# Optimization experiments

Measured on AMD Instinct MI355X. Metric: run time of the kernel, lower is better.

## Reference

```python
import jax, jax.numpy as jnp
import numpy as np

# LABEL2ID assumed: O=0, B-PERSON=1, I-PERSON=2 (standard tagset ordering)
B_ID = 1
I_ID = 2
SMOOTH = 1e-5
B_WEIGHT = 3.0
I_END_WEIGHT = 2.5
CONTEXT_WEIGHT = 1.5
N_TOKENS = 8388608
NUM_CLASSES = 9


def setup_inputs() -> dict:
    key = jax.random.key(0)
    k1, k2 = jax.random.split(key)
    inputs = jax.random.normal(k1, (N_TOKENS, NUM_CLASSES), dtype=jnp.float32)
    targets = jax.random.randint(k2, (N_TOKENS,), 0, NUM_CLASSES)
    return {"inputs": inputs, "targets": targets}


def _boundary_weights(t):
    # base weight 1; B-PERSON -> b_weight
    w = jnp.ones(t.shape, jnp.float32)
    w = jnp.where(t == B_ID, B_WEIGHT, w)
    # I-PERSON followed by non-I-PERSON -> i_end_weight
    # (torch pads shifted with the last element, so the final I is never flagged here)
    nxt_dup = jnp.concatenate([t[1:], t[-1:]])
    w = jnp.where((t == I_ID) & (nxt_dup != I_ID), I_END_WEIGHT, w)
    # token immediately before a B-PERSON -> context_weight (overwrites prior weights,
    # matching torch's later scatter assignment; index -1 for a leading B is filtered out)
    nxt0 = jnp.concatenate([t[1:], jnp.zeros((1,), t.dtype)])
    w = jnp.where(nxt0 == B_ID, CONTEXT_WEIGHT, w)
    return w


def reference(inputs, targets):
    probs = jax.nn.softmax(inputs, axis=1)                      # [N, C]
    one_hot = jax.nn.one_hot(targets, NUM_CLASSES, dtype=jnp.float32)
    w = _boundary_weights(targets)[:, None]                     # [N, 1]
    intersection = jnp.sum(probs * one_hot * w, axis=0)         # [C]
    denominator = jnp.sum(probs * w, axis=0) + jnp.sum(one_hot * w, axis=0)
    dice_coef = (2.0 * intersection + SMOOTH) / (denominator + SMOOTH)
    return 1.0 - dice_coef.mean()
```

## Files before the change

### kernel.cpp

```cpp
#include <hip/hip_runtime.h>

#define NC 9
#define BLOCK 256
#define TPT 4
#define CHUNK (BLOCK * TPT)
#define GRID 2048


__global__ __launch_bounds__(BLOCK) void dice_partial(
    const float* __restrict__ logits,
    const int*   __restrict__ targets,
    float*       __restrict__ partials,
    int n)
{
    float sWP[NC], sI[NC], sOH[NC];
    #pragma unroll
    for (int c = 0; c < NC; ++c) { sWP[c] = 0.f; sI[c] = 0.f; sOH[c] = 0.f; }

    const int tid = threadIdx.x;
    const int nChunks = (n + CHUNK - 1) / CHUNK;

    for (int chunk = blockIdx.x; chunk < nChunks; chunk += gridDim.x) {
        const int base = chunk * CHUNK + tid * TPT;

        if (base + TPT <= n) {
            const float4* g4 = reinterpret_cast<const float4*>(logits + (size_t)base * NC);
            float f[TPT * NC];
            #pragma unroll
            for (int k = 0; k < 9; ++k) {
                const float4 q = g4[k];
                f[4 * k]     = q.x;
                f[4 * k + 1] = q.y;
                f[4 * k + 2] = q.z;
                f[4 * k + 3] = q.w;
            }
            const int4 t4 = *reinterpret_cast<const int4*>(targets + base);
            int tg[TPT];
            tg[0] = t4.x; tg[1] = t4.y; tg[2] = t4.z; tg[3] = t4.w;
            const int  tExtra = (base + TPT < n) ? targets[base + TPT] : 0;
            const bool lastIsGlobalEnd = (base + TPT == n);

            #pragma unroll
            for (int j = 0; j < TPT; ++j) {
                const int  t    = tg[j];
                const bool last = (j == TPT - 1) && lastIsGlobalEnd;
                const int  tn   = (j < TPT - 1) ? tg[j + 1] : tExtra;

                float w = 1.0f;
                if (t == 1) w = 3.0f;
                const int nxt_dup = last ? t : tn;
                if (t == 2 && nxt_dup != 2) w = 2.5f;
                if (!last && tn == 1) w = 1.5f;

                float v[NC];
                float s = 0.f;
                #pragma unroll
                for (int c = 0; c < NC; ++c) { v[c] = __expf(f[j * NC + c]); s += v[c]; }
                const float inv = __builtin_amdgcn_rcpf(s);

                #pragma unroll
                for (int c = 0; c < NC; ++c) {
                    const float p   = v[c] * inv;
                    const bool  hit = (t == c);
                    sWP[c] += w * p;
                    sI[c]  += hit ? w * p : 0.f;
                    sOH[c] += hit ? w : 0.f;
                }
            }
        } else {
            for (int j = 0; j < TPT; ++j) {
                const int a = base + j;
                if (a >= n) break;
                const int  t    = targets[a];
                const bool last = (a == n - 1);
                const int  tn   = last ? 0 : targets[a + 1];

                float w = 1.0f;
                if (t == 1) w = 3.0f;
                const int nxt_dup = last ? t : tn;
                if (t == 2 && nxt_dup != 2) w = 2.5f;
                if (!last && tn == 1) w = 1.5f;

                float v[NC];
                float s = 0.f;
                #pragma unroll
                for (int c = 0; c < NC; ++c) { v[c] = __expf(logits[(size_t)a * NC + c]); s += v[c]; }
                const float inv = __builtin_amdgcn_rcpf(s);

                #pragma unroll
                for (int c = 0; c < NC; ++c) {
                    const float p   = v[c] * inv;
                    const bool  hit = (t == c);
                    sWP[c] += w * p;
                    sI[c]  += hit ? w * p : 0.f;
                    sOH[c] += hit ? w : 0.f;
                }
            }
        }
    }

    #pragma unroll
    for (int off = 32; off; off >>= 1) {
        #pragma unroll
        for (int c = 0; c < NC; ++c) {
            sWP[c] += __shfl_down(sWP[c], off);
            sI[c]  += __shfl_down(sI[c], off);
            sOH[c] += __shfl_down(sOH[c], off);
        }
    }

    __shared__ float red[4][32];
    const int lane = tid & 63;
    const int wid  = tid >> 6;
    if (lane == 0) {
        #pragma unroll
        for (int c = 0; c < NC; ++c) {
            red[wid][c]      = sWP[c];
            red[wid][9 + c]  = sI[c];
            red[wid][18 + c] = sOH[c];
        }
    }
    __syncthreads();
    if (tid < 27) {
        partials[blockIdx.x * 32 + tid] =
            red[0][tid] + red[1][tid] + red[2][tid] + red[3][tid];
    }
}

__global__ __launch_bounds__(1024) void dice_reduce(
    const float* __restrict__ partials,
    float*       __restrict__ out,
    int nblocks)
{
    const int c = threadIdx.x & 31;
    const int r = threadIdx.x >> 5;
    float s = 0.f;
    if (c < 27) {
        for (int b = r; b < nblocks; b += 32)
            s += partials[b * 32 + c];
    }
    __shared__ float acc[32][33];
    acc[r][c] = s;
    __syncthreads();

    __shared__ float A[32];
    if (threadIdx.x < 32) {
        float tot = 0.f;
        #pragma unroll
        for (int k = 0; k < 32; ++k) tot += acc[k][threadIdx.x];
        A[threadIdx.x] = tot;
    }
    __syncthreads();
    if (threadIdx.x == 0) {
        float dsum = 0.f;
        #pragma unroll
        for (int cc = 0; cc < NC; ++cc) {
            const float inter = A[9 + cc];
            const float den   = A[cc] + A[18 + cc];
            dsum += (2.f * inter + 1e-5f) / (den + 1e-5f);
        }
        out[0] = 1.f - dsum * (1.f / 9.f);
    }
}

extern "C" void kernel_launch(void* const* d_in, const int* in_sizes, int n_in,
                              void* d_out, int out_size, void* d_ws, size_t ws_size,
                              hipStream_t stream)
{
    const float* logits   = (const float*)d_in[0];
    const int*   targets  = (const int*)d_in[1];
    float*       out      = (float*)d_out;
    float*       partials = (float*)d_ws;
    const int n = in_sizes[1];

    const int nChunks = (n + CHUNK - 1) / CHUNK;
    const int grid = nChunks < GRID ? nChunks : GRID;
    dice_partial<<<grid, BLOCK, 0, stream>>>(logits, targets, partials, n);
    dice_reduce<<<1, 1024, 0, stream>>>(partials, out, grid);
}
```

Baseline: 78.82 us.

## Stage logits through LDS with coalesced loads and register double-buffering

Each block is reduced to a single 64-thread wavefront that loads 256 tokens' logits as perfectly coalesced float4s (lane-strided) into registers, stores them to LDS, then reads them back per-thread in token-contiguous order. The next chunk's global loads are issued before computing the current chunk, giving software prefetch in two register sets. This replaces strided per-thread 144-byte vector loads, which coalesce poorly, and removes the cross-wave shared reduction and barrier. It trades higher register pressure and fewer threads per block, which may lower latency hiding, and the grid stays capped at 2048 single-wave blocks.

```diff
diff --git a/kernel.cpp b/kernel.cpp
--- a/kernel.cpp
+++ b/kernel.cpp
@@ -1,101 +1,121 @@
 #include <hip/hip_runtime.h>
 
 #define NC 9
-#define BLOCK 256
-#define TPT 4
-#define CHUNK (BLOCK * TPT)
+#define TPW 256
+#define F4PW (TPW * NC / 4)
 #define GRID 2048
 
 
-__global__ __launch_bounds__(BLOCK) void dice_partial(
+__global__ __launch_bounds__(64) void dice_partial(
     const float* __restrict__ logits,
     const int*   __restrict__ targets,
     float*       __restrict__ partials,
     int n)
 {
+    __shared__ __align__(16) float4 buf[2][F4PW];
+    __shared__ float red[32];
+
     float sWP[NC], sI[NC], sOH[NC];
     #pragma unroll
     for (int c = 0; c < NC; ++c) { sWP[c] = 0.f; sI[c] = 0.f; sOH[c] = 0.f; }
 
-    const int tid = threadIdx.x;
-    const int nChunks = (n + CHUNK - 1) / CHUNK;
+    const int l = threadIdx.x;
+    const int G = gridDim.x;
+    const int nFull = n / TPW;
 
-    for (int chunk = blockIdx.x; chunk < nChunks; chunk += gridDim.x) {
-        const int base = chunk * CHUNK + tid * TPT;
+    const float4* gbase = reinterpret_cast<const float4*>(logits);
 
-        if (base + TPT <= n) {
-            const float4* g4 = reinterpret_cast<const float4*>(logits + (size_t)base * NC);
-            float f[TPT * NC];
-            #pragma unroll
-            for (int k = 0; k < 9; ++k) {
-                const float4 q = g4[k];
-                f[4 * k]     = q.x;
-                f[4 * k + 1] = q.y;
-                f[4 * k + 2] = q.z;
-                f[4 * k + 3] = q.w;
-            }
-            const int4 t4 = *reinterpret_cast<const int4*>(targets + base);
-            int tg[TPT];
-            tg[0] = t4.x; tg[1] = t4.y; tg[2] = t4.z; tg[3] = t4.w;
-            const int  tExtra = (base + TPT < n) ? targets[base + TPT] : 0;
-            const bool lastIsGlobalEnd = (base + TPT == n);
+    float4 tA0,tA1,tA2,tA3,tA4,tA5,tA6,tA7,tA8;
+    float4 tB0,tB1,tB2,tB3,tB4,tB5,tB6,tB7,tB8;
 
-            #pragma unroll
-            for (int j = 0; j < TPT; ++j) {
-                const int  t    = tg[j];
-                const bool last = (j == TPT - 1) && lastIsGlobalEnd;
-                const int  tn   = (j < TPT - 1) ? tg[j + 1] : tExtra;
+#define LOADT(dst, c)  do { const float4* g4 = gbase + (size_t)(c) * F4PW; \
+        dst##0 = g4[0*64+l]; dst##1 = g4[1*64+l]; dst##2 = g4[2*64+l]; \
+        dst##3 = g4[3*64+l]; dst##4 = g4[4*64+l]; dst##5 = g4[5*64+l]; \
+        dst##6 = g4[6*64+l]; dst##7 = g4[7*64+l]; dst##8 = g4[8*64+l]; } while(0)
 
-                float w = 1.0f;
-                if (t == 1) w = 3.0f;
-                const int nxt_dup = last ? t : tn;
-                if (t == 2 && nxt_dup != 2) w = 2.5f;
-                if (!last && tn == 1) w = 1.5f;
+#define STORET(p, src) do { float4* B = &buf[p][0]; \
+        B[0*64+l]=src##0; B[1*64+l]=src##1; B[2*64+l]=src##2; \
+        B[3*64+l]=src##3; B[4*64+l]=src##4; B[5*64+l]=src##5; \
+        B[6*64+l]=src##6; B[7*64+l]=src##7; B[8*64+l]=src##8; } while(0)
 
-                float v[NC];
-                float s = 0.f;
-                #pragma unroll
-                for (int c = 0; c < NC; ++c) { v[c] = __expf(f[j * NC + c]); s += v[c]; }
-                const float inv = __builtin_amdgcn_rcpf(s);
+#define COMPUTE(p, cch) do {                                                  \
+        float f[4 * NC];                                                      \
+        _Pragma("unroll")                                                     \
+        for (int k = 0; k < 9; ++k) {                                         \
+            const float4 q = buf[p][l * 9 + k];                               \
+            f[4*k] = q.x; f[4*k+1] = q.y; f[4*k+2] = q.z; f[4*k+3] = q.w;     \
+        }                                                                     \
+        const int tok0 = (cch) * TPW + l * 4;                                 \
+        const int4 t4 = *reinterpret_cast<const int4*>(targets + tok0);       \
+        int tg[4]; tg[0]=t4.x; tg[1]=t4.y; tg[2]=t4.z; tg[3]=t4.w;            \
+        const int  tExtra = (tok0 + 4 < n) ? targets[tok0 + 4] : 0;           \
+        const bool lastIsEnd = (tok0 + 4 == n);                               \
+        _Pragma("unroll")                                                     \
+        for (int j = 0; j < 4; ++j) {                                         \
+            const int  t    = tg[j];                                          \
+            const bool last = (j == 3) && lastIsEnd;                          \
+            const int  tn   = (j < 3) ? tg[j + 1] : tExtra;                   \
+            float w = 1.0f;                                                   \
+            if (t == 1) w = 3.0f;                                             \
+            const int nxt_dup = last ? t : tn;                                \
+            if (t == 2 && nxt_dup != 2) w = 2.5f;                             \
+            if (!last && tn == 1) w = 1.5f;                                   \
+            float v[NC]; float s = 0.f;                                       \
+            _Pragma("unroll")                                                 \
+            for (int c = 0; c < NC; ++c) { v[c] = __expf(f[j*NC+c]); s += v[c]; } \
+            const float inv = __builtin_amdgcn_rcpf(s);                       \
+            _Pragma("unroll")                                                 \
+            for (int c = 0; c < NC; ++c) {                                    \
+                const float p_ = v[c] * inv;                                  \
+                const bool hit = (t == c);                                    \
+                sWP[c] += w * p_;                                             \
+                sI[c]  += hit ? w * p_ : 0.f;                                 \
+                sOH[c] += hit ? w : 0.f;                                      \
+            }                                                                 \
+        }                                                                     \
+    } while(0)
 
-                #pragma unroll
-                for (int c = 0; c < NC; ++c) {
-                    const float p   = v[c] * inv;
-                    const bool  hit = (t == c);
-                    sWP[c] += w * p;
-                    sI[c]  += hit ? w * p : 0.f;
-                    sOH[c] += hit ? w : 0.f;
-                }
-            }
-        } else {
-            for (int j = 0; j < TPT; ++j) {
-                const int a = base + j;
-                if (a >= n) break;
-                const int  t    = targets[a];
-                const bool last = (a == n - 1);
-                const int  tn   = last ? 0 : targets[a + 1];
+    int c0 = blockIdx.x;
+    if (c0 < nFull) LOADT(tA, c0);
 
-                float w = 1.0f;
-                if (t == 1) w = 3.0f;
-                const int nxt_dup = last ? t : tn;
-                if (t == 2 && nxt_dup != 2) w = 2.5f;
-                if (!last && tn == 1) w = 1.5f;
+    while (c0 < nFull) {
+        STORET(0, tA);
+        {
+            const int c1 = c0 + G;
+            if (c1 < nFull) LOADT(tB, c1);
+            COMPUTE(0, c0);
+            c0 = c1;
+        }
+        if (c0 >= nFull) break;
+        STORET(1, tB);
+        {
+            const int c2 = c0 + G;
+            if (c2 < nFull) LOADT(tA, c2);
+            COMPUTE(1, c0);
+            c0 = c2;
+        }
+    }
 
-                float v[NC];
-                float s = 0.f;
-                #pragma unroll
-                for (int c = 0; c < NC; ++c) { v[c] = __expf(logits[(size_t)a * NC + c]); s += v[c]; }
-                const float inv = __builtin_amdgcn_rcpf(s);
-
-                #pragma unroll
-                for (int c = 0; c < NC; ++c) {
-                    const float p   = v[c] * inv;
-                    const bool  hit = (t == c);
-                    sWP[c] += w * p;
-                    sI[c]  += hit ? w * p : 0.f;
-                    sOH[c] += hit ? w : 0.f;
-                }
-            }
+    for (int a = nFull * TPW + blockIdx.x * 64 + l; a < n; a += G * 64) {
+        const int  t    = targets[a];
+        const bool last = (a == n - 1);
+        const int  tn   = last ? 0 : targets[a + 1];
+        float w = 1.0f;
+        if (t == 1) w = 3.0f;
+        const int nxt_dup = last ? t : tn;
+        if (t == 2 && nxt_dup != 2) w = 2.5f;
+        if (!last && tn == 1) w = 1.5f;
+        float v[NC]; float s = 0.f;
+        #pragma unroll
+        for (int c = 0; c < NC; ++c) { v[c] = __expf(logits[(size_t)a * NC + c]); s += v[c]; }
+        const float inv = __builtin_amdgcn_rcpf(s);
+        #pragma unroll
+        for (int c = 0; c < NC; ++c) {
+            const float p = v[c] * inv;
+            const bool hit = (t == c);
+            sWP[c] += w * p;
+            sI[c]  += hit ? w * p : 0.f;
+            sOH[c] += hit ? w : 0.f;
         }
     }
 
@@ -109,22 +129,16 @@
         }
     }
 
-    __shared__ float red[4][32];
-    const int lane = tid & 63;
-    const int wid  = tid >> 6;
-    if (lane == 0) {
+    if (l == 0) {
         #pragma unroll
         for (int c = 0; c < NC; ++c) {
-            red[wid][c]      = sWP[c];
-            red[wid][9 + c]  = sI[c];
-            red[wid][18 + c] = sOH[c];
+            red[c]      = sWP[c];
+            red[9 + c]  = sI[c];
+            red[18 + c] = sOH[c];
         }
     }
-    __syncthreads();
-    if (tid < 27) {
-        partials[blockIdx.x * 32 + tid] =
-            red[0][tid] + red[1][tid] + red[2][tid] + red[3][tid];
-    }
+    __builtin_amdgcn_s_waitcnt(0);
+    if (l < 27) partials[blockIdx.x * 32 + l] = red[l];
 }
 
 __global__ __launch_bounds__(1024) void dice_reduce(
@@ -173,8 +187,9 @@
     float*       partials = (float*)d_ws;
     const int n = in_sizes[1];
 
-    const int nChunks = (n + CHUNK - 1) / CHUNK;
+    int nChunks = (n + TPW - 1) / TPW;
+    if (nChunks < 1) nChunks = 1;
     const int grid = nChunks < GRID ? nChunks : GRID;
-    dice_partial<<<grid, BLOCK, 0, stream>>>(logits, targets, partials, n);
+    dice_partial<<<grid, 64, 0, stream>>>(logits, targets, partials, n);
     dice_reduce<<<1, 1024, 0, stream>>>(partials, out, grid);
 }
```

After: 81.12 us. +2.9%, slower.
